# Kernel tuning notes

Hardware: AMD Instinct MI355X
Metric: run time of the kernel (lower is better)

## Reference

```python
import jax, jax.numpy as jnp
import numpy as np

DM, DFF = 128, 512          # d_model, d_ff = 4*d_model
B, D, L, FACTOR = 8, 64, 256, 10  # batch, ts_d, seg_num, router factor


def _ln(x, g, b):
    m = jnp.mean(x, axis=-1, keepdims=True)
    v = jnp.mean(jnp.square(x - m), axis=-1, keepdims=True)
    return (x - m) * jax.lax.rsqrt(v + 1e-5) * g + b


def _mlp(x, W1, b1, W2, b2):
    # nn.Linear -> GELU(exact/erf, torch default) -> nn.Linear
    return jax.nn.gelu(x @ W1 + b1, approximate=False) @ W2 + b2


def setup_inputs():
    key = jax.random.key(0)
    ks = jax.random.split(key, 9)
    f32 = jnp.float32
    return {
        "x": jax.random.normal(ks[0], (B, D, L, DM), f32),
        "router": jax.random.normal(ks[1], (L, FACTOR, DM), f32),
        # out_projection biases of the three AutoCorrelationLayers
        "bo_time": jax.random.normal(ks[2], (DM,), f32) * 0.02,
        "bo_send": jax.random.normal(ks[3], (DM,), f32) * 0.02,
        "bo_recv": jax.random.normal(ks[4], (DM,), f32) * 0.02,
        "g1": jnp.ones((DM,), f32), "be1": jnp.zeros((DM,), f32),
        "g2": jnp.ones((DM,), f32), "be2": jnp.zeros((DM,), f32),
        "g3": jnp.ones((DM,), f32), "be3": jnp.zeros((DM,), f32),
        "g4": jnp.ones((DM,), f32), "be4": jnp.zeros((DM,), f32),
        "W1a": jax.random.normal(ks[5], (DM, DFF), f32) * 0.02, "b1a": jnp.zeros((DFF,), f32),
        "W2a": jax.random.normal(ks[6], (DFF, DM), f32) * 0.02, "b2a": jnp.zeros((DM,), f32),
        "W1b": jax.random.normal(ks[7], (DM, DFF), f32) * 0.02, "b1b": jnp.zeros((DFF,), f32),
        "W2b": jax.random.normal(ks[8], (DFF, DM), f32) * 0.02, "b2b": jnp.zeros((DM,), f32),
    }


def reference(x, router, bo_time, bo_send, bo_recv, g1, be1, g2, be2, g3, be3, g4, be4,
              W1a, b1a, W2a, b2a, W1b, b1b, W2b, b2b):
    b, d, l, dm = x.shape
    time_in = x.reshape(b * d, l, dm)
    # FourierBlock is constructed with modes=0 -> get_frequency_modes returns an
    # EMPTY index set -> out_ft stays all-zero -> irfft(0) == 0. Therefore every
    # AutoCorrelationLayer output is exactly its out_projection bias broadcast;
    # the Q/K/V/out weights, bo_send and the router are dead w.r.t. the output
    # (zero gradient). Dropout is identity in eval mode.
    dim_in = _ln(time_in + bo_time, g1, be1)                            # residual + norm1
    dim_in = _ln(dim_in + _mlp(dim_in, W1a, b1a, W2a, b2a), g2, be2)    # MLP1 + norm2
    # '(b d) l dm -> (b l) d dm'
    dim_send = dim_in.reshape(b, d, l, dm).transpose(0, 2, 1, 3).reshape(b * l, d, dm)
    dim_enc = _ln(dim_send + bo_recv, g3, be3)                          # dim_receiver bias + norm3
    dim_enc = _ln(dim_enc + _mlp(dim_enc, W1b, b1b, W2b, b2b), g4, be4) # MLP2 + norm4
    # '(b l) d dm -> b d l dm'
    return dim_enc.reshape(b, l, d, dm).transpose(0, 2, 1, 3)
```

## Files before the change

kernel.cpp:

```cpp
#include <hip/hip_runtime.h>
#include <hip/hip_fp16.h>

typedef _Float16 f16;
typedef f16 f16x8 __attribute__((ext_vector_type(8)));
typedef f16 f16x4 __attribute__((ext_vector_type(4)));
typedef f16 f16x2 __attribute__((ext_vector_type(2)));
typedef float f32x4 __attribute__((ext_vector_type(4)));

#define DM 128
#define DFF 512

__device__ __align__(16) f16 g_wimg[524288];

__device__ __forceinline__ int swz(int row, int k2 ) {
  return row * 256 + (k2 ^ ((row & 7) << 4));
}

__device__ __forceinline__ float gelu_f(float x) {
  float z = fabsf(x) * 0.70710678118654752f;
  float t = __builtin_amdgcn_rcpf(fmaf(0.3275911f, z, 1.0f));
  float p = fmaf(1.061405429f, t, -1.453152027f);
  p = fmaf(p, t, 1.421413741f);
  p = fmaf(p, t, -0.284496736f);
  p = fmaf(p, t, 0.254829592f);
  p = p * t;
  float e = __expf(-z * z);
  float er = fmaf(-p, e, 1.0f);
  er = copysignf(er, x);
  return 0.5f * x * (1.0f + er);
}

__global__ __launch_bounds__(256) void prep_weights(
    const float* __restrict__ W1a, const float* __restrict__ W2a,
    const float* __restrict__ W1b, const float* __restrict__ W2b) {
  int p = blockIdx.x * 256 + threadIdx.x;
  int mat = p >> 16;
  int rem = p & 65535;
  int plane = rem >> 15;
  int rem2 = rem & 32767;
  int frag = rem2 >> 8;
  int q = rem2 & 255;
  int lane = q >> 2;
  int j = (q & 3) * 2;
  int chunk = frag >> 5;
  int cb = (frag >> 2) & 7;
  int ks = frag & 3;
  int l15 = lane & 15, l4 = lane >> 4;
  int col16 = cb * 16 + l15;
  int kk = ks * 32 + l4 * 8 + j;
  const float* W = (mat == 0) ? W1a : (mat == 1) ? W2a : (mat == 2) ? W1b : W2b;
  float s0, s1;
  if ((mat & 1) == 0) {
    int colg = chunk * 128 + col16;
    s0 = W[kk * 512 + colg];
    s1 = W[(kk + 1) * 512 + colg];
  } else {
    int kg = chunk * 128 + kk;
    s0 = W[kg * 128 + col16];
    s1 = W[(kg + 1) * 128 + col16];
  }
  f16x2 h;
  if (plane == 0) {
    h.x = (f16)s0;
    h.y = (f16)s1;
  } else {
    h.x = (f16)(s0 - (float)(f16)s0);
    h.y = (f16)(s1 - (float)(f16)s1);
  }
  *(f16x2*)((unsigned char*)g_wimg + mat * 262144 + plane * 131072 +
            frag * 1024 + lane * 16 + j * 2) = h;
}

__device__ __forceinline__ void run_mlp(
    const f16x8 (&afh)[2][4], const f16x8 (&afl)[2][4], f32x4 (&zacc)[2][4],
    const f16* __restrict__ Wimg1, const f16* __restrict__ Wimg2,
    const float* __restrict__ b1,
    unsigned char* shh, unsigned char* shl,
    int wr, int wc, int l15, int l4, int lane) {
  for (int chunk = 0; chunk < 4; ++chunk) {
    const f16* b1h = Wimg1 + chunk * 16384;
    const f16* b1l = Wimg1 + 65536 + chunk * 16384;
    f32x4 t[2][4];
#pragma unroll
    for (int ri = 0; ri < 2; ++ri)
#pragma unroll
      for (int ci = 0; ci < 4; ++ci) t[ri][ci] = (f32x4){0.f, 0.f, 0.f, 0.f};
#pragma unroll
    for (int ks = 0; ks < 4; ++ks) {
#pragma unroll
      for (int ci = 0; ci < 4; ++ci) {
        int cb = wc * 4 + ci;
        const int fo = ((cb * 4 + ks) * 64 + lane) * 8;
        f16x8 bh = *(const f16x8*)(b1h + fo);
        f16x8 bl = *(const f16x8*)(b1l + fo);
        t[0][ci] = __builtin_amdgcn_mfma_f32_16x16x32_f16(afh[0][ks], bh, t[0][ci], 0, 0, 0);
        t[1][ci] = __builtin_amdgcn_mfma_f32_16x16x32_f16(afh[1][ks], bh, t[1][ci], 0, 0, 0);
        t[0][ci] = __builtin_amdgcn_mfma_f32_16x16x32_f16(afl[0][ks], bh, t[0][ci], 0, 0, 0);
        t[1][ci] = __builtin_amdgcn_mfma_f32_16x16x32_f16(afl[1][ks], bh, t[1][ci], 0, 0, 0);
        t[0][ci] = __builtin_amdgcn_mfma_f32_16x16x32_f16(afh[0][ks], bl, t[0][ci], 0, 0, 0);
        t[1][ci] = __builtin_amdgcn_mfma_f32_16x16x32_f16(afh[1][ks], bl, t[1][ci], 0, 0, 0);
      }
    }
    __syncthreads();
#pragma unroll
    for (int ci = 0; ci < 4; ++ci) {
      int cl = wc * 64 + ci * 16 + l15;
      float bias = b1[chunk * 128 + cl];
#pragma unroll
      for (int ri = 0; ri < 2; ++ri)
#pragma unroll
        for (int r = 0; r < 4; ++r) {
          int row = 32 * wr + 16 * ri + l4 * 4 + r;
          float g = gelu_f(t[ri][ci][r] + bias);
          f16 gh = (f16)g;
          *(f16*)(shh + swz(row, 2 * cl)) = gh;
          *(f16*)(shl + swz(row, 2 * cl)) = (f16)(g - (float)gh);
        }
    }
    __syncthreads();
    const f16* b2h = Wimg2 + chunk * 16384;
    const f16* b2l = Wimg2 + 65536 + chunk * 16384;
    f16x8 a2h[2][4], a2l[2][4];
#pragma unroll
    for (int ri = 0; ri < 2; ++ri)
#pragma unroll
      for (int ks = 0; ks < 4; ++ks) {
        int row = 32 * wr + 16 * ri + l15;
        int off = swz(row, 2 * (ks * 32 + l4 * 8));
        a2h[ri][ks] = *(const f16x8*)(shh + off);
        a2l[ri][ks] = *(const f16x8*)(shl + off);
      }
#pragma unroll
    for (int ks = 0; ks < 4; ++ks) {
#pragma unroll
      for (int ci = 0; ci < 4; ++ci) {
        int cb = wc * 4 + ci;
        const int fo = ((cb * 4 + ks) * 64 + lane) * 8;
        f16x8 bh = *(const f16x8*)(b2h + fo);
        f16x8 bl = *(const f16x8*)(b2l + fo);
        zacc[0][ci] = __builtin_amdgcn_mfma_f32_16x16x32_f16(a2h[0][ks], bh, zacc[0][ci], 0, 0, 0);
        zacc[1][ci] = __builtin_amdgcn_mfma_f32_16x16x32_f16(a2h[1][ks], bh, zacc[1][ci], 0, 0, 0);
        zacc[0][ci] = __builtin_amdgcn_mfma_f32_16x16x32_f16(a2l[0][ks], bh, zacc[0][ci], 0, 0, 0);
        zacc[1][ci] = __builtin_amdgcn_mfma_f32_16x16x32_f16(a2l[1][ks], bh, zacc[1][ci], 0, 0, 0);
        zacc[0][ci] = __builtin_amdgcn_mfma_f32_16x16x32_f16(a2h[0][ks], bl, zacc[0][ci], 0, 0, 0);
        zacc[1][ci] = __builtin_amdgcn_mfma_f32_16x16x32_f16(a2h[1][ks], bl, zacc[1][ci], 0, 0, 0);
      }
    }
  }
}

__global__ __launch_bounds__(256) void tsal_kernel(
    const float* __restrict__ x,
    const float* __restrict__ bo_time, const float* __restrict__ bo_recv,
    const float* __restrict__ g1, const float* __restrict__ be1,
    const float* __restrict__ g2, const float* __restrict__ be2,
    const float* __restrict__ g3, const float* __restrict__ be3,
    const float* __restrict__ g4, const float* __restrict__ be4,
    const float* __restrict__ b1a, const float* __restrict__ b2a,
    const float* __restrict__ b1b, const float* __restrict__ b2b,
    float* __restrict__ out) {
  __shared__ __align__(16) unsigned char smem[34816];
  unsigned char* shh = smem;
  unsigned char* shl = smem + 16384;
  float2* red1 = (float2*)(smem + 32768);
  float2* red2 = (float2*)(smem + 33792);

  const int tid = threadIdx.x;
  const int lane = tid & 63;
  const int wv = tid >> 6;
  const int wr = wv >> 1, wc = wv & 1;
  const int l15 = lane & 15, l4 = lane >> 4;
  const int row0 = blockIdx.x * 64;

#pragma unroll
  for (int it = 0; it < 8; ++it) {
    int rl = wv * 16 + it * 2 + (lane >> 5);
    int c0 = (lane & 31) * 4;
    float4 xv = *(const float4*)(x + (size_t)(row0 + rl) * 128 + c0);
    float4 bt = *(const float4*)(bo_time + c0);
    float vx = xv.x + bt.x, vy = xv.y + bt.y, vz = xv.z + bt.z, vw = xv.w + bt.w;
    float s = vx + vy + vz + vw;
    float q = vx * vx + vy * vy + vz * vz + vw * vw;
#pragma unroll
    for (int m = 16; m >= 1; m >>= 1) {
      s += __shfl_xor(s, m, 64);
      q += __shfl_xor(q, m, 64);
    }
    float mm = s * (1.f / 128.f);
    float rs = rsqrtf(q * (1.f / 128.f) - mm * mm + 1e-5f);
    float4 gv = *(const float4*)(g1 + c0);
    float4 bv = *(const float4*)(be1 + c0);
    float w0 = (vx - mm) * rs * gv.x + bv.x;
    float w1 = (vy - mm) * rs * gv.y + bv.y;
    float w2 = (vz - mm) * rs * gv.z + bv.z;
    float w3 = (vw - mm) * rs * gv.w + bv.w;
    int off = rl * 256 + ((c0 * 2) ^ ((rl & 7) << 4));
    f16x4 hv, lv;
    hv.x = (f16)w0; hv.y = (f16)w1; hv.z = (f16)w2; hv.w = (f16)w3;
    lv.x = (f16)(w0 - (float)hv.x);
    lv.y = (f16)(w1 - (float)hv.y);
    lv.z = (f16)(w2 - (float)hv.z);
    lv.w = (f16)(w3 - (float)hv.w);
    *(f16x4*)(shh + off) = hv;
    *(f16x4*)(shl + off) = lv;
  }
  __syncthreads();

  f16x8 afh[2][4], afl[2][4];
#pragma unroll
  for (int ri = 0; ri < 2; ++ri)
#pragma unroll
    for (int ks = 0; ks < 4; ++ks) {
      int row = 32 * wr + 16 * ri + l15;
      int off = swz(row, 2 * (ks * 32 + l4 * 8));
      afh[ri][ks] = *(const f16x8*)(shh + off);
      afl[ri][ks] = *(const f16x8*)(shl + off);
    }
  f32x4 zacc[2][4];
#pragma unroll
  for (int ri = 0; ri < 2; ++ri)
#pragma unroll
    for (int ci = 0; ci < 4; ++ci)
#pragma unroll
      for (int r = 0; r < 4; ++r) {
        int row = 32 * wr + 16 * ri + l4 * 4 + r;
        int col = wc * 64 + ci * 16 + l15;
        int off = swz(row, 2 * col);
        zacc[ri][ci][r] = (float)(*(const f16*)(shh + off)) +
                          (float)(*(const f16*)(shl + off));
      }

  run_mlp(afh, afl, zacc, g_wimg, g_wimg + 131072, b1a, shh, shl, wr, wc, l15, l4, lane);

#pragma unroll
  for (int ci = 0; ci < 4; ++ci) {
    float bb = b2a[wc * 64 + ci * 16 + l15];
#pragma unroll
    for (int ri = 0; ri < 2; ++ri)
#pragma unroll
      for (int r = 0; r < 4; ++r) zacc[ri][ci][r] += bb;
  }
#pragma unroll
  for (int ri = 0; ri < 2; ++ri)
#pragma unroll
    for (int r = 0; r < 4; ++r) {
      float s = 0.f, q = 0.f;
#pragma unroll
      for (int ci = 0; ci < 4; ++ci) {
        float v = zacc[ri][ci][r];
        s += v; q += v * v;
      }
#pragma unroll
      for (int m = 8; m >= 1; m >>= 1) {
        s += __shfl_xor(s, m, 64);
        q += __shfl_xor(q, m, 64);
      }
      if (l15 == 0) red1[(32 * wr + 16 * ri + l4 * 4 + r) * 2 + wc] = make_float2(s, q);
    }
  __syncthreads();
  float g2v[4], be2v[4], brv[4];
#pragma unroll
  for (int ci = 0; ci < 4; ++ci) {
    int col = wc * 64 + ci * 16 + l15;
    g2v[ci] = g2[col]; be2v[ci] = be2[col]; brv[ci] = bo_recv[col];
  }
#pragma unroll
  for (int ri = 0; ri < 2; ++ri)
#pragma unroll
    for (int r = 0; r < 4; ++r) {
      int row = 32 * wr + 16 * ri + l4 * 4 + r;
      float2 pa = red1[row * 2 + 0], pb = red1[row * 2 + 1];
      float mm = (pa.x + pb.x) * (1.f / 128.f);
      float var = (pa.y + pb.y) * (1.f / 128.f) - mm * mm;
      float rs = rsqrtf(var + 1e-5f);
      float s = 0.f, q = 0.f;
#pragma unroll
      for (int ci = 0; ci < 4; ++ci) {
        float zn = (zacc[ri][ci][r] - mm) * rs * g2v[ci] + be2v[ci];
        float t3 = zn + brv[ci];
        zacc[ri][ci][r] = t3;
        s += t3; q += t3 * t3;
      }
#pragma unroll
      for (int m = 8; m >= 1; m >>= 1) {
        s += __shfl_xor(s, m, 64);
        q += __shfl_xor(q, m, 64);
      }
      if (l15 == 0) red2[row * 2 + wc] = make_float2(s, q);
    }
  __syncthreads();
  float g3v[4], be3v[4];
#pragma unroll
  for (int ci = 0; ci < 4; ++ci) {
    int col = wc * 64 + ci * 16 + l15;
    g3v[ci] = g3[col]; be3v[ci] = be3[col];
  }
#pragma unroll
  for (int ri = 0; ri < 2; ++ri)
#pragma unroll
    for (int r = 0; r < 4; ++r) {
      int row = 32 * wr + 16 * ri + l4 * 4 + r;
      float2 pa = red2[row * 2 + 0], pb = red2[row * 2 + 1];
      float mm = (pa.x + pb.x) * (1.f / 128.f);
      float var = (pa.y + pb.y) * (1.f / 128.f) - mm * mm;
      float rs = rsqrtf(var + 1e-5f);
#pragma unroll
      for (int ci = 0; ci < 4; ++ci) {
        int col = wc * 64 + ci * 16 + l15;
        float y = (zacc[ri][ci][r] - mm) * rs * g3v[ci] + be3v[ci];
        zacc[ri][ci][r] = y;
        f16 yh = (f16)y;
        *(f16*)(shh + swz(row, 2 * col)) = yh;
        *(f16*)(shl + swz(row, 2 * col)) = (f16)(y - (float)yh);
      }
    }
  __syncthreads();
#pragma unroll
  for (int ri = 0; ri < 2; ++ri)
#pragma unroll
    for (int ks = 0; ks < 4; ++ks) {
      int row = 32 * wr + 16 * ri + l15;
      int off = swz(row, 2 * (ks * 32 + l4 * 8));
      afh[ri][ks] = *(const f16x8*)(shh + off);
      afl[ri][ks] = *(const f16x8*)(shl + off);
    }

  run_mlp(afh, afl, zacc, g_wimg + 262144, g_wimg + 393216, b1b, shh, shl, wr, wc, l15, l4, lane);

#pragma unroll
  for (int ci = 0; ci < 4; ++ci) {
    float bb = b2b[wc * 64 + ci * 16 + l15];
#pragma unroll
    for (int ri = 0; ri < 2; ++ri)
#pragma unroll
      for (int r = 0; r < 4; ++r) zacc[ri][ci][r] += bb;
  }
#pragma unroll
  for (int ri = 0; ri < 2; ++ri)
#pragma unroll
    for (int r = 0; r < 4; ++r) {
      float s = 0.f, q = 0.f;
#pragma unroll
      for (int ci = 0; ci < 4; ++ci) {
        float v = zacc[ri][ci][r];
        s += v; q += v * v;
      }
#pragma unroll
      for (int m = 8; m >= 1; m >>= 1) {
        s += __shfl_xor(s, m, 64);
        q += __shfl_xor(q, m, 64);
      }
      if (l15 == 0) red1[(32 * wr + 16 * ri + l4 * 4 + r) * 2 + wc] = make_float2(s, q);
    }
  __syncthreads();
  float g4v[4], be4v[4];
#pragma unroll
  for (int ci = 0; ci < 4; ++ci) {
    int col = wc * 64 + ci * 16 + l15;
    g4v[ci] = g4[col]; be4v[ci] = be4[col];
  }
#pragma unroll
  for (int ri = 0; ri < 2; ++ri)
#pragma unroll
    for (int r = 0; r < 4; ++r) {
      int row = 32 * wr + 16 * ri + l4 * 4 + r;
      float2 pa = red1[row * 2 + 0], pb = red1[row * 2 + 1];
      float mm = (pa.x + pb.x) * (1.f / 128.f);
      float var = (pa.y + pb.y) * (1.f / 128.f) - mm * mm;
      float rs = rsqrtf(var + 1e-5f);
#pragma unroll
      for (int ci = 0; ci < 4; ++ci) {
        int col = wc * 64 + ci * 16 + l15;
        float o = (zacc[ri][ci][r] - mm) * rs * g4v[ci] + be4v[ci];
        out[(size_t)(row0 + row) * 128 + col] = o;
      }
    }
}

extern "C" void kernel_launch(void* const* d_in, const int* in_sizes, int n_in,
                              void* d_out, int out_size, void* d_ws, size_t ws_size,
                              hipStream_t stream) {
  const float* x = (const float*)d_in[0];
  const float* bo_time = (const float*)d_in[2];
  const float* bo_recv = (const float*)d_in[4];
  const float* g1 = (const float*)d_in[5];
  const float* be1 = (const float*)d_in[6];
  const float* g2 = (const float*)d_in[7];
  const float* be2 = (const float*)d_in[8];
  const float* g3 = (const float*)d_in[9];
  const float* be3 = (const float*)d_in[10];
  const float* g4 = (const float*)d_in[11];
  const float* be4 = (const float*)d_in[12];
  const float* W1a = (const float*)d_in[13];
  const float* b1a = (const float*)d_in[14];
  const float* W2a = (const float*)d_in[15];
  const float* b2a = (const float*)d_in[16];
  const float* W1b = (const float*)d_in[17];
  const float* b1b = (const float*)d_in[18];
  const float* W2b = (const float*)d_in[19];
  const float* b2b = (const float*)d_in[20];
  float* outp = (float*)d_out;

  int nrows = in_sizes[0] / 128;
  prep_weights<<<1024, 256, 0, stream>>>(W1a, W2a, W1b, W2b);
  tsal_kernel<<<nrows / 64, 256, 0, stream>>>(
      x, bo_time, bo_recv, g1, be1, g2, be2, g3, be3, g4, be4,
      b1a, b2a, b1b, b2b, outp);
}
```

Measured before the change: 682.2 us.

## Give each wave its own 16 rows and drop block-wide barriers

Restructures the fused MLP kernel so each wave processes 16 full rows across all 128 columns. Activations stay fp32 in a per-wave padded LDS scratch and are split into hi/lo halves on the fly. This removes every __syncthreads and the cross-wave LayerNorm reduction through shared memory, which now becomes in-wave shuffles. The first GEMM is transposed (weights as the A operand), and launch bounds request two blocks per CU. The cost is that each wave now reads the full weight image instead of half, roughly doubling weight fetches, and register pressure rises with 8 accumulator tiles.

```diff
diff --git a/kernel.cpp b/kernel.cpp
--- a/kernel.cpp
+++ b/kernel.cpp
@@ -3,18 +3,12 @@
 
 typedef _Float16 f16;
 typedef f16 f16x8 __attribute__((ext_vector_type(8)));
-typedef f16 f16x4 __attribute__((ext_vector_type(4)));
 typedef f16 f16x2 __attribute__((ext_vector_type(2)));
 typedef float f32x4 __attribute__((ext_vector_type(4)));
 
-#define DM 128
-#define DFF 512
-
 __device__ __align__(16) f16 g_wimg[524288];
 
-__device__ __forceinline__ int swz(int row, int k2 ) {
-  return row * 256 + (k2 ^ ((row & 7) << 4));
-}
+#define RSTRIDE 528
 
 __device__ __forceinline__ float gelu_f(float x) {
   float z = fabsf(x) * 0.70710678118654752f;
@@ -71,85 +65,82 @@
             frag * 1024 + lane * 16 + j * 2) = h;
 }
 
-__device__ __forceinline__ void run_mlp(
-    const f16x8 (&afh)[2][4], const f16x8 (&afl)[2][4], f32x4 (&zacc)[2][4],
-    const f16* __restrict__ Wimg1, const f16* __restrict__ Wimg2,
-    const float* __restrict__ b1,
-    unsigned char* shh, unsigned char* shl,
-    int wr, int wc, int l15, int l4, int lane) {
+__device__ __forceinline__ void split8(const float4& a, const float4& b,
+                                       f16x8& h, f16x8& l) {
+  float v[8] = {a.x, a.y, a.z, a.w, b.x, b.y, b.z, b.w};
+#pragma unroll
+  for (int j = 0; j < 8; ++j) {
+    f16 x = (f16)v[j];
+    h[j] = x;
+    l[j] = (f16)(v[j] - (float)x);
+  }
+}
+
+__device__ __forceinline__ void mlp_stage(
+    char* scr, const f16x8 (&bfh)[4], const f16x8 (&bfl)[4], f32x4 (&zacc)[8],
+    const f16* __restrict__ W1img, const f16* __restrict__ W2img,
+    const float* __restrict__ b1, int lane, int l15, int l4) {
   for (int chunk = 0; chunk < 4; ++chunk) {
-    const f16* b1h = Wimg1 + chunk * 16384;
-    const f16* b1l = Wimg1 + 65536 + chunk * 16384;
-    f32x4 t[2][4];
-#pragma unroll
-    for (int ri = 0; ri < 2; ++ri)
-#pragma unroll
-      for (int ci = 0; ci < 4; ++ci) t[ri][ci] = (f32x4){0.f, 0.f, 0.f, 0.f};
+#pragma unroll
+    for (int m = 0; m < 8; ++m) {
+      f32x4 t4 = {0.f, 0.f, 0.f, 0.f};
+#pragma unroll
+      for (int ks = 0; ks < 4; ++ks) {
+        int frag = (chunk * 8 + m) * 4 + ks;
+        f16x8 wh = *(const f16x8*)(W1img + frag * 512 + lane * 8);
+        f16x8 wl = *(const f16x8*)(W1img + 65536 + frag * 512 + lane * 8);
+        t4 = __builtin_amdgcn_mfma_f32_16x16x32_f16(wh, bfh[ks], t4, 0, 0, 0);
+        t4 = __builtin_amdgcn_mfma_f32_16x16x32_f16(wl, bfh[ks], t4, 0, 0, 0);
+        t4 = __builtin_amdgcn_mfma_f32_16x16x32_f16(wh, bfl[ks], t4, 0, 0, 0);
+      }
+      float4 bv = *(const float4*)(b1 + chunk * 128 + m * 16 + l4 * 4);
+      float4 g;
+      g.x = gelu_f(t4[0] + bv.x);
+      g.y = gelu_f(t4[1] + bv.y);
+      g.z = gelu_f(t4[2] + bv.z);
+      g.w = gelu_f(t4[3] + bv.w);
+      *(float4*)(scr + l15 * RSTRIDE + m * 64 + l4 * 16) = g;
+    }
 #pragma unroll
     for (int ks = 0; ks < 4; ++ks) {
-#pragma unroll
-      for (int ci = 0; ci < 4; ++ci) {
-        int cb = wc * 4 + ci;
-        const int fo = ((cb * 4 + ks) * 64 + lane) * 8;
-        f16x8 bh = *(const f16x8*)(b1h + fo);
-        f16x8 bl = *(const f16x8*)(b1l + fo);
-        t[0][ci] = __builtin_amdgcn_mfma_f32_16x16x32_f16(afh[0][ks], bh, t[0][ci], 0, 0, 0);
-        t[1][ci] = __builtin_amdgcn_mfma_f32_16x16x32_f16(afh[1][ks], bh, t[1][ci], 0, 0, 0);
-        t[0][ci] = __builtin_amdgcn_mfma_f32_16x16x32_f16(afl[0][ks], bh, t[0][ci], 0, 0, 0);
-        t[1][ci] = __builtin_amdgcn_mfma_f32_16x16x32_f16(afl[1][ks], bh, t[1][ci], 0, 0, 0);
-        t[0][ci] = __builtin_amdgcn_mfma_f32_16x16x32_f16(afh[0][ks], bl, t[0][ci], 0, 0, 0);
-        t[1][ci] = __builtin_amdgcn_mfma_f32_16x16x32_f16(afh[1][ks], bl, t[1][ci], 0, 0, 0);
+      const char* hb = scr + l15 * RSTRIDE + ks * 128 + l4 * 32;
+      float4 h0 = *(const float4*)(hb);
+      float4 h1 = *(const float4*)(hb + 16);
+      f16x8 ah, al;
+      split8(h0, h1, ah, al);
+#pragma unroll
+      for (int n = 0; n < 8; ++n) {
+        int frag = (chunk * 8 + n) * 4 + ks;
+        f16x8 bh = *(const f16x8*)(W2img + frag * 512 + lane * 8);
+        f16x8 bl = *(const f16x8*)(W2img + 65536 + frag * 512 + lane * 8);
+        zacc[n] = __builtin_amdgcn_mfma_f32_16x16x32_f16(ah, bh, zacc[n], 0, 0, 0);
+        zacc[n] = __builtin_amdgcn_mfma_f32_16x16x32_f16(al, bh, zacc[n], 0, 0, 0);
+        zacc[n] = __builtin_amdgcn_mfma_f32_16x16x32_f16(ah, bl, zacc[n], 0, 0, 0);
       }
     }
-    __syncthreads();
-#pragma unroll
-    for (int ci = 0; ci < 4; ++ci) {
-      int cl = wc * 64 + ci * 16 + l15;
-      float bias = b1[chunk * 128 + cl];
-#pragma unroll
-      for (int ri = 0; ri < 2; ++ri)
-#pragma unroll
-        for (int r = 0; r < 4; ++r) {
-          int row = 32 * wr + 16 * ri + l4 * 4 + r;
-          float g = gelu_f(t[ri][ci][r] + bias);
-          f16 gh = (f16)g;
-          *(f16*)(shh + swz(row, 2 * cl)) = gh;
-          *(f16*)(shl + swz(row, 2 * cl)) = (f16)(g - (float)gh);
-        }
-    }
-    __syncthreads();
-    const f16* b2h = Wimg2 + chunk * 16384;
-    const f16* b2l = Wimg2 + 65536 + chunk * 16384;
-    f16x8 a2h[2][4], a2l[2][4];
-#pragma unroll
-    for (int ri = 0; ri < 2; ++ri)
-#pragma unroll
-      for (int ks = 0; ks < 4; ++ks) {
-        int row = 32 * wr + 16 * ri + l15;
-        int off = swz(row, 2 * (ks * 32 + l4 * 8));
-        a2h[ri][ks] = *(const f16x8*)(shh + off);
-        a2l[ri][ks] = *(const f16x8*)(shl + off);
-      }
-#pragma unroll
-    for (int ks = 0; ks < 4; ++ks) {
-#pragma unroll
-      for (int ci = 0; ci < 4; ++ci) {
-        int cb = wc * 4 + ci;
-        const int fo = ((cb * 4 + ks) * 64 + lane) * 8;
-        f16x8 bh = *(const f16x8*)(b2h + fo);
-        f16x8 bl = *(const f16x8*)(b2l + fo);
-        zacc[0][ci] = __builtin_amdgcn_mfma_f32_16x16x32_f16(a2h[0][ks], bh, zacc[0][ci], 0, 0, 0);
-        zacc[1][ci] = __builtin_amdgcn_mfma_f32_16x16x32_f16(a2h[1][ks], bh, zacc[1][ci], 0, 0, 0);
-        zacc[0][ci] = __builtin_amdgcn_mfma_f32_16x16x32_f16(a2l[0][ks], bh, zacc[0][ci], 0, 0, 0);
-        zacc[1][ci] = __builtin_amdgcn_mfma_f32_16x16x32_f16(a2l[1][ks], bh, zacc[1][ci], 0, 0, 0);
-        zacc[0][ci] = __builtin_amdgcn_mfma_f32_16x16x32_f16(a2h[0][ks], bl, zacc[0][ci], 0, 0, 0);
-        zacc[1][ci] = __builtin_amdgcn_mfma_f32_16x16x32_f16(a2h[1][ks], bl, zacc[1][ci], 0, 0, 0);
-      }
-    }
-  }
-}
-
-__global__ __launch_bounds__(256) void tsal_kernel(
+  }
+}
+
+#define ROW_LN_STATS(ZACC, MMV, RSV)                                   \
+  float MMV[4], RSV[4];                                                \
+  _Pragma("unroll") for (int r = 0; r < 4; ++r) {                      \
+    float s = 0.f, q = 0.f;                                            \
+    _Pragma("unroll") for (int n = 0; n < 8; ++n) {                    \
+      float v = ZACC[n][r];                                            \
+      s += v;                                                          \
+      q += v * v;                                                      \
+    }                                                                  \
+    _Pragma("unroll") for (int m = 8; m >= 1; m >>= 1) {               \
+      s += __shfl_xor(s, m, 64);                                       \
+      q += __shfl_xor(q, m, 64);                                       \
+    }                                                                  \
+    float mm = s * (1.f / 128.f);                                      \
+    float var = q * (1.f / 128.f) - mm * mm;                           \
+    MMV[r] = mm;                                                       \
+    RSV[r] = rsqrtf(var + 1e-5f);                                      \
+  }
+
+__global__ __launch_bounds__(256, 2) void tsal_kernel(
     const float* __restrict__ x,
     const float* __restrict__ bo_time, const float* __restrict__ bo_recv,
     const float* __restrict__ g1, const float* __restrict__ be1,
@@ -159,24 +150,20 @@
     const float* __restrict__ b1a, const float* __restrict__ b2a,
     const float* __restrict__ b1b, const float* __restrict__ b2b,
     float* __restrict__ out) {
-  __shared__ __align__(16) unsigned char smem[34816];
-  unsigned char* shh = smem;
-  unsigned char* shl = smem + 16384;
-  float2* red1 = (float2*)(smem + 32768);
-  float2* red2 = (float2*)(smem + 33792);
+  __shared__ __align__(16) char smem[33792];
 
   const int tid = threadIdx.x;
   const int lane = tid & 63;
   const int wv = tid >> 6;
-  const int wr = wv >> 1, wc = wv & 1;
   const int l15 = lane & 15, l4 = lane >> 4;
-  const int row0 = blockIdx.x * 64;
+  char* scr = smem + wv * 8448;
+  const int R0 = blockIdx.x * 64 + wv * 16;
 
 #pragma unroll
   for (int it = 0; it < 8; ++it) {
-    int rl = wv * 16 + it * 2 + (lane >> 5);
+    int rl = it * 2 + (lane >> 5);
     int c0 = (lane & 31) * 4;
-    float4 xv = *(const float4*)(x + (size_t)(row0 + rl) * 128 + c0);
+    float4 xv = *(const float4*)(x + (size_t)(R0 + rl) * 128 + c0);
     float4 bt = *(const float4*)(bo_time + c0);
     float vx = xv.x + bt.x, vy = xv.y + bt.y, vz = xv.z + bt.z, vw = xv.w + bt.w;
     float s = vx + vy + vz + vw;
@@ -190,191 +177,102 @@
     float rs = rsqrtf(q * (1.f / 128.f) - mm * mm + 1e-5f);
     float4 gv = *(const float4*)(g1 + c0);
     float4 bv = *(const float4*)(be1 + c0);
-    float w0 = (vx - mm) * rs * gv.x + bv.x;
-    float w1 = (vy - mm) * rs * gv.y + bv.y;
-    float w2 = (vz - mm) * rs * gv.z + bv.z;
-    float w3 = (vw - mm) * rs * gv.w + bv.w;
-    int off = rl * 256 + ((c0 * 2) ^ ((rl & 7) << 4));
-    f16x4 hv, lv;
-    hv.x = (f16)w0; hv.y = (f16)w1; hv.z = (f16)w2; hv.w = (f16)w3;
-    lv.x = (f16)(w0 - (float)hv.x);
-    lv.y = (f16)(w1 - (float)hv.y);
-    lv.z = (f16)(w2 - (float)hv.z);
-    lv.w = (f16)(w3 - (float)hv.w);
-    *(f16x4*)(shh + off) = hv;
-    *(f16x4*)(shl + off) = lv;
-  }
-  __syncthreads();
-
-  f16x8 afh[2][4], afl[2][4];
-#pragma unroll
-  for (int ri = 0; ri < 2; ++ri)
-#pragma unroll
-    for (int ks = 0; ks < 4; ++ks) {
-      int row = 32 * wr + 16 * ri + l15;
-      int off = swz(row, 2 * (ks * 32 + l4 * 8));
-      afh[ri][ks] = *(const f16x8*)(shh + off);
-      afl[ri][ks] = *(const f16x8*)(shl + off);
-    }
-  f32x4 zacc[2][4];
-#pragma unroll
-  for (int ri = 0; ri < 2; ++ri)
-#pragma unroll
-    for (int ci = 0; ci < 4; ++ci)
+    float4 w;
+    w.x = (vx - mm) * rs * gv.x + bv.x;
+    w.y = (vy - mm) * rs * gv.y + bv.y;
+    w.z = (vz - mm) * rs * gv.z + bv.z;
+    w.w = (vw - mm) * rs * gv.w + bv.w;
+    *(float4*)(scr + rl * RSTRIDE + c0 * 4) = w;
+  }
+
+  f16x8 bfh[4], bfl[4];
+#pragma unroll
+  for (int ks = 0; ks < 4; ++ks) {
+    const char* wb = scr + l15 * RSTRIDE + ks * 128 + l4 * 32;
+    float4 a0 = *(const float4*)(wb);
+    float4 a1 = *(const float4*)(wb + 16);
+    split8(a0, a1, bfh[ks], bfl[ks]);
+  }
+  f32x4 zacc[8];
+#pragma unroll
+  for (int n = 0; n < 8; ++n)
+#pragma unroll
+    for (int r = 0; r < 4; ++r)
+      zacc[n][r] = *(const float*)(scr + (l4 * 4 + r) * RSTRIDE +
+                                   (n * 16 + l15) * 4);
+
+  mlp_stage(scr, bfh, bfl, zacc, g_wimg, g_wimg + 131072, b1a, lane, l15, l4);
+
+  float b2v[8], g2v[8], be2v[8], brv[8], g3v[8], be3v[8];
+#pragma unroll
+  for (int n = 0; n < 8; ++n) {
+    int col = n * 16 + l15;
+    b2v[n] = b2a[col];
+    g2v[n] = g2[col];
+    be2v[n] = be2[col];
+    brv[n] = bo_recv[col];
+    g3v[n] = g3[col];
+    be3v[n] = be3[col];
+  }
+#pragma unroll
+  for (int n = 0; n < 8; ++n)
+#pragma unroll
+    for (int r = 0; r < 4; ++r) zacc[n][r] += b2v[n];
+  {
+    ROW_LN_STATS(zacc, mm2, rs2)
+#pragma unroll
+    for (int n = 0; n < 8; ++n)
+#pragma unroll
+      for (int r = 0; r < 4; ++r)
+        zacc[n][r] = (zacc[n][r] - mm2[r]) * rs2[r] * g2v[n] + be2v[n] + brv[n];
+  }
+  {
+    ROW_LN_STATS(zacc, mm3, rs3)
+#pragma unroll
+    for (int n = 0; n < 8; ++n)
+#pragma unroll
+      for (int r = 0; r < 4; ++r)
+        zacc[n][r] = (zacc[n][r] - mm3[r]) * rs3[r] * g3v[n] + be3v[n];
+  }
+#pragma unroll
+  for (int n = 0; n < 8; ++n)
+#pragma unroll
+    for (int r = 0; r < 4; ++r)
+      *(float*)(scr + (l4 * 4 + r) * RSTRIDE + (n * 16 + l15) * 4) =
+          zacc[n][r];
+#pragma unroll
+  for (int ks = 0; ks < 4; ++ks) {
+    const char* yb = scr + l15 * RSTRIDE + ks * 128 + l4 * 32;
+    float4 a0 = *(const float4*)(yb);
+    float4 a1 = *(const float4*)(yb + 16);
+    split8(a0, a1, bfh[ks], bfl[ks]);
+  }
+
+  mlp_stage(scr, bfh, bfl, zacc, g_wimg + 262144, g_wimg + 393216, b1b, lane,
+            l15, l4);
+
+  float b4v[8], g4v[8], be4v[8];
+#pragma unroll
+  for (int n = 0; n < 8; ++n) {
+    int col = n * 16 + l15;
+    b4v[n] = b2b[col];
+    g4v[n] = g4[col];
+    be4v[n] = be4[col];
+  }
+#pragma unroll
+  for (int n = 0; n < 8; ++n)
+#pragma unroll
+    for (int r = 0; r < 4; ++r) zacc[n][r] += b4v[n];
+  {
+    ROW_LN_STATS(zacc, mm4, rs4)
+#pragma unroll
+    for (int n = 0; n < 8; ++n)
 #pragma unroll
       for (int r = 0; r < 4; ++r) {
-        int row = 32 * wr + 16 * ri + l4 * 4 + r;
-        int col = wc * 64 + ci * 16 + l15;
-        int off = swz(row, 2 * col);
-        zacc[ri][ci][r] = (float)(*(const f16*)(shh + off)) +
-                          (float)(*(const f16*)(shl + off));
+        float o = (zacc[n][r] - mm4[r]) * rs4[r] * g4v[n] + be4v[n];
+        out[(size_t)(R0 + l4 * 4 + r) * 128 + n * 16 + l15] = o;
       }
-
-  run_mlp(afh, afl, zacc, g_wimg, g_wimg + 131072, b1a, shh, shl, wr, wc, l15, l4, lane);
-
-#pragma unroll
-  for (int ci = 0; ci < 4; ++ci) {
-    float bb = b2a[wc * 64 + ci * 16 + l15];
-#pragma unroll
-    for (int ri = 0; ri < 2; ++ri)
-#pragma unroll
-      for (int r = 0; r < 4; ++r) zacc[ri][ci][r] += bb;
-  }
-#pragma unroll
-  for (int ri = 0; ri < 2; ++ri)
-#pragma unroll
-    for (int r = 0; r < 4; ++r) {
-      float s = 0.f, q = 0.f;
-#pragma unroll
-      for (int ci = 0; ci < 4; ++ci) {
-        float v = zacc[ri][ci][r];
-        s += v; q += v * v;
-      }
-#pragma unroll
-      for (int m = 8; m >= 1; m >>= 1) {
-        s += __shfl_xor(s, m, 64);
-        q += __shfl_xor(q, m, 64);
-      }
-      if (l15 == 0) red1[(32 * wr + 16 * ri + l4 * 4 + r) * 2 + wc] = make_float2(s, q);
-    }
-  __syncthreads();
-  float g2v[4], be2v[4], brv[4];
-#pragma unroll
-  for (int ci = 0; ci < 4; ++ci) {
-    int col = wc * 64 + ci * 16 + l15;
-    g2v[ci] = g2[col]; be2v[ci] = be2[col]; brv[ci] = bo_recv[col];
-  }
-#pragma unroll
-  for (int ri = 0; ri < 2; ++ri)
-#pragma unroll
-    for (int r = 0; r < 4; ++r) {
-      int row = 32 * wr + 16 * ri + l4 * 4 + r;
-      float2 pa = red1[row * 2 + 0], pb = red1[row * 2 + 1];
-      float mm = (pa.x + pb.x) * (1.f / 128.f);
-      float var = (pa.y + pb.y) * (1.f / 128.f) - mm * mm;
-      float rs = rsqrtf(var + 1e-5f);
-      float s = 0.f, q = 0.f;
-#pragma unroll
-      for (int ci = 0; ci < 4; ++ci) {
-        float zn = (zacc[ri][ci][r] - mm) * rs * g2v[ci] + be2v[ci];
-        float t3 = zn + brv[ci];
-        zacc[ri][ci][r] = t3;
-        s += t3; q += t3 * t3;
-      }
-#pragma unroll
-      for (int m = 8; m >= 1; m >>= 1) {
-        s += __shfl_xor(s, m, 64);
-        q += __shfl_xor(q, m, 64);
-      }
-      if (l15 == 0) red2[row * 2 + wc] = make_float2(s, q);
-    }
-  __syncthreads();
-  float g3v[4], be3v[4];
-#pragma unroll
-  for (int ci = 0; ci < 4; ++ci) {
-    int col = wc * 64 + ci * 16 + l15;
-    g3v[ci] = g3[col]; be3v[ci] = be3[col];
-  }
-#pragma unroll
-  for (int ri = 0; ri < 2; ++ri)
-#pragma unroll
-    for (int r = 0; r < 4; ++r) {
-      int row = 32 * wr + 16 * ri + l4 * 4 + r;
-      float2 pa = red2[row * 2 + 0], pb = red2[row * 2 + 1];
-      float mm = (pa.x + pb.x) * (1.f / 128.f);
-      float var = (pa.y + pb.y) * (1.f / 128.f) - mm * mm;
-      float rs = rsqrtf(var + 1e-5f);
-#pragma unroll
-      for (int ci = 0; ci < 4; ++ci) {
-        int col = wc * 64 + ci * 16 + l15;
-        float y = (zacc[ri][ci][r] - mm) * rs * g3v[ci] + be3v[ci];
-        zacc[ri][ci][r] = y;
-        f16 yh = (f16)y;
-        *(f16*)(shh + swz(row, 2 * col)) = yh;
-        *(f16*)(shl + swz(row, 2 * col)) = (f16)(y - (float)yh);
-      }
-    }
-  __syncthreads();
-#pragma unroll
-  for (int ri = 0; ri < 2; ++ri)
-#pragma unroll
-    for (int ks = 0; ks < 4; ++ks) {
-      int row = 32 * wr + 16 * ri + l15;
-      int off = swz(row, 2 * (ks * 32 + l4 * 8));
-      afh[ri][ks] = *(const f16x8*)(shh + off);
-      afl[ri][ks] = *(const f16x8*)(shl + off);
-    }
-
-  run_mlp(afh, afl, zacc, g_wimg + 262144, g_wimg + 393216, b1b, shh, shl, wr, wc, l15, l4, lane);
-
-#pragma unroll
-  for (int ci = 0; ci < 4; ++ci) {
-    float bb = b2b[wc * 64 + ci * 16 + l15];
-#pragma unroll
-    for (int ri = 0; ri < 2; ++ri)
-#pragma unroll
-      for (int r = 0; r < 4; ++r) zacc[ri][ci][r] += bb;
-  }
-#pragma unroll
-  for (int ri = 0; ri < 2; ++ri)
-#pragma unroll
-    for (int r = 0; r < 4; ++r) {
-      float s = 0.f, q = 0.f;
-#pragma unroll
-      for (int ci = 0; ci < 4; ++ci) {
-        float v = zacc[ri][ci][r];
-        s += v; q += v * v;
-      }
-#pragma unroll
-      for (int m = 8; m >= 1; m >>= 1) {
-        s += __shfl_xor(s, m, 64);
-        q += __shfl_xor(q, m, 64);
-      }
-      if (l15 == 0) red1[(32 * wr + 16 * ri + l4 * 4 + r) * 2 + wc] = make_float2(s, q);
-    }
-  __syncthreads();
-  float g4v[4], be4v[4];
-#pragma unroll
-  for (int ci = 0; ci < 4; ++ci) {
-    int col = wc * 64 + ci * 16 + l15;
-    g4v[ci] = g4[col]; be4v[ci] = be4[col];
-  }
-#pragma unroll
-  for (int ri = 0; ri < 2; ++ri)
-#pragma unroll
-    for (int r = 0; r < 4; ++r) {
-      int row = 32 * wr + 16 * ri + l4 * 4 + r;
-      float2 pa = red1[row * 2 + 0], pb = red1[row * 2 + 1];
-      float mm = (pa.x + pb.x) * (1.f / 128.f);
-      float var = (pa.y + pb.y) * (1.f / 128.f) - mm * mm;
-      float rs = rsqrtf(var + 1e-5f);
-#pragma unroll
-      for (int ci = 0; ci < 4; ++ci) {
-        int col = wc * 64 + ci * 16 + l15;
-        float o = (zacc[ri][ci][r] - mm) * rs * g4v[ci] + be4v[ci];
-        out[(size_t)(row0 + row) * 128 + col] = o;
-      }
-    }
+  }
 }
 
 extern "C" void kernel_launch(void* const* d_in, const int* in_sizes, int n_in,
@@ -391,14 +289,14 @@
   const float* be3 = (const float*)d_in[10];
   const float* g4 = (const float*)d_in[11];
   const float* be4 = (const float*)d_in[12];
+  const float* b1a = (const float*)d_in[14];
+  const float* b2a = (const float*)d_in[16];
+  const float* b1b = (const float*)d_in[18];
+  const float* b2b = (const float*)d_in[20];
   const float* W1a = (const float*)d_in[13];
-  const float* b1a = (const float*)d_in[14];
   const float* W2a = (const float*)d_in[15];
-  const float* b2a = (const float*)d_in[16];
   const float* W1b = (const float*)d_in[17];
-  const float* b1b = (const float*)d_in[18];
   const float* W2b = (const float*)d_in[19];
-  const float* b2b = (const float*)d_in[20];
   float* outp = (float*)d_out;
 
   int nrows = in_sizes[0] / 128;
```

Result: faster. 654.7 us (-4.0%).
